# Optimization experiments

Measured on AMD Instinct MI355X. Metric: run time of the kernel, lower is better.

## Reference

```python
import jax, jax.numpy as jnp
import numpy as np

NUM_STEPS = 3  # matches init_kwargs num_steps
UNITS = 256
N_STRUCT = 4096
N_ATOMS_TOTAL = 131072
FEAT_IN = 256


def setup_inputs() -> dict:
    key = jax.random.key(0)
    ks = jax.random.split(key, 7)
    field = jax.random.normal(ks[0], (N_ATOMS_TOTAL, FEAT_IN), dtype=jnp.float32)
    # Dense(units) params
    Wd = jax.random.normal(ks[1], (FEAT_IN, UNITS), dtype=jnp.float32) / np.sqrt(FEAT_IN)
    bd = jnp.zeros((UNITS,), dtype=jnp.float32)
    # Keras LSTM params: kernel [2*units, 4*units], recurrent [units, 4*units], bias [4*units]
    Wk = jax.random.normal(ks[2], (2 * UNITS, 4 * UNITS), dtype=jnp.float32) / np.sqrt(2 * UNITS)
    Wr = jax.random.normal(ks[3], (UNITS, 4 * UNITS), dtype=jnp.float32) / np.sqrt(UNITS)
    b_lstm = jnp.zeros((4 * UNITS,), dtype=jnp.float32)
    # sorted segment ids = get_segment_indices_from_n(counts)
    segment_ids = jnp.sort(jax.random.randint(ks[4], (N_ATOMS_TOTAL,), 0, N_STRUCT)).astype(jnp.int32)
    return {"field": field, "Wd": Wd, "bd": bd, "Wk": Wk, "Wr": Wr,
            "b_lstm": b_lstm, "segment_ids": segment_ids, "n_struct": N_STRUCT}


def _segment_softmax(e, seg, num_segments):
    # per-channel softmax within each segment (matches unsorted_segment_softmax)
    m = jax.ops.segment_max(e, seg, num_segments=num_segments)
    ex = jnp.exp(e - m[seg])
    s = jax.ops.segment_sum(ex, seg, num_segments=num_segments)
    return ex / s[seg]


def _lstm_step(x, h, c, Wk, Wr, b):
    # Keras gate order: i, f, g(c), o
    z = x @ Wk + h @ Wr + b
    i, f, g, o = jnp.split(z, 4, axis=-1)
    c_new = jax.nn.sigmoid(f) * c + jax.nn.sigmoid(i) * jnp.tanh(g)
    h_new = jax.nn.sigmoid(o) * jnp.tanh(c_new)
    return h_new, c_new


def reference(field, Wd, bd, Wk, Wr, b_lstm, segment_ids, n_struct):
    units = Wd.shape[1]
    x = field @ Wd + bd                              # [N_atoms, units]
    q_star = jnp.zeros((n_struct, 2 * units), dtype=x.dtype)
    h = jnp.zeros((n_struct, units), dtype=x.dtype)
    c = jnp.zeros((n_struct, units), dtype=x.dtype)
    for _ in range(NUM_STEPS):
        h, c = _lstm_step(q_star, h, c, Wk, Wr, b_lstm)
        qt = h                                        # [n_struct, units]
        eit = x * qt[segment_ids]                     # gather == tf.repeat(qt, counts)
        ait = _segment_softmax(eit, segment_ids, n_struct)
        rt = jax.ops.segment_sum(ait * x, segment_ids, num_segments=n_struct)
        q_star = jnp.concatenate([qt, rt], axis=-1)   # [n_struct, 2*units]
    return q_star
```

## Files before the change

kernel.cpp:

```cpp
#include <hip/hip_runtime.h>
#include <math.h>

#define N_ATOMS   131072
#define FEAT      256
#define UNITS     256
#define NSTRUCT   4096
#define ZDIM      1024
#define QDIM      512
#define KLSTM     768

typedef __attribute__((ext_vector_type(8))) __bf16 bf16x8;
typedef __attribute__((ext_vector_type(4))) float  f32x4;

__device__ __forceinline__ float sigm(float v) { return 1.0f / (1.0f + __expf(-v)); }

__device__ __forceinline__ unsigned short bf16_rne(float v) {
    unsigned int u = __float_as_uint(v);
    u += 0x7fffu + ((u >> 16) & 1u);
    return (unsigned short)(u >> 16);
}
__device__ __forceinline__ float bf16_f32(unsigned short b) {
    return __uint_as_float(((unsigned int)b) << 16);
}
__device__ __forceinline__ bf16x8 frag_ld(const unsigned short* p) {
    uint4 u = *(const uint4*)p;
    bf16x8 r; __builtin_memcpy(&r, &u, 16); return r;
}

__global__ void seg_offs_kernel(const int* __restrict__ seg, int* __restrict__ offs) {
    int s = blockIdx.x * blockDim.x + threadIdx.x;
    if (s > NSTRUCT) return;
    int lo = 0, hi = N_ATOMS;
    while (lo < hi) {
        int mid = (lo + hi) >> 1;
        if (seg[mid] < s) lo = mid + 1; else hi = mid;
    }
    offs[s] = lo;
}

__global__ __launch_bounds__(256) void prep_wd_kernel(
    const float* __restrict__ Wd, unsigned short* __restrict__ Th,
    unsigned short* __restrict__ Tl)
{
    int t = blockIdx.x * 256 + threadIdx.x;
    int k = t >> 8, n = t & 255;
    float v = Wd[t];
    unsigned short h = bf16_rne(v);
    unsigned short l = bf16_rne(v - bf16_f32(h));
    Th[n * FEAT + k] = h;
    Tl[n * FEAT + k] = l;
}

__global__ __launch_bounds__(256) void prep_wlstm_kernel(
    const float* __restrict__ Wk, const float* __restrict__ Wr,
    unsigned short* __restrict__ Th, unsigned short* __restrict__ Tl)
{
    int t = blockIdx.x * 256 + threadIdx.x;
    int k = t >> 10, n = t & 1023;
    float v = (k < QDIM) ? Wk[t] : Wr[t - QDIM * ZDIM];
    unsigned short h = bf16_rne(v);
    unsigned short l = bf16_rne(v - bf16_f32(h));
    Th[n * KLSTM + k] = h;
    Tl[n * KLSTM + k] = l;
}

__global__ __launch_bounds__(256) void gemm_x_mfma(
    const float* __restrict__ A,
    const unsigned short* __restrict__ BTh,
    const unsigned short* __restrict__ BTl,
    const float* __restrict__ bias, float* __restrict__ C)
{
    __shared__ unsigned short Ah[128][32], Al[128][32], Bh[128][32], Bl[128][32];
    const int bn = blockIdx.x * 128;
    const int bm = blockIdx.y * 128;
    const int t  = threadIdx.x;
    const int w  = t >> 6, l = t & 63;
    const int wr = w & 1, wc = w >> 1;
    const int lm = l & 15, koff = (l >> 4) * 8;

    f32x4 acc[4][4] = {};

    for (int k0 = 0; k0 < FEAT; k0 += 32) {
        #pragma unroll
        for (int i = 0; i < 4; ++i) {
            int flat = t + i * 256;
            int m = flat >> 3, kq = flat & 7;
            const float4 v = *(const float4*)&A[(size_t)(bm + m) * FEAT + k0 + kq * 4];
            unsigned short h0 = bf16_rne(v.x), h1 = bf16_rne(v.y);
            unsigned short h2 = bf16_rne(v.z), h3 = bf16_rne(v.w);
            unsigned short l0 = bf16_rne(v.x - bf16_f32(h0));
            unsigned short l1 = bf16_rne(v.y - bf16_f32(h1));
            unsigned short l2 = bf16_rne(v.z - bf16_f32(h2));
            unsigned short l3 = bf16_rne(v.w - bf16_f32(h3));
            uint2 hw, lw;
            hw.x = (unsigned)h0 | ((unsigned)h1 << 16);
            hw.y = (unsigned)h2 | ((unsigned)h3 << 16);
            lw.x = (unsigned)l0 | ((unsigned)l1 << 16);
            lw.y = (unsigned)l2 | ((unsigned)l3 << 16);
            *(uint2*)&Ah[m][kq * 4] = hw;
            *(uint2*)&Al[m][kq * 4] = lw;
        }
        #pragma unroll
        for (int i = 0; i < 2; ++i) {
            int flat = t + i * 256;
            int n = flat >> 2, kc = flat & 3;
            *(uint4*)&Bh[n][kc * 8] = *(const uint4*)&BTh[(size_t)(bn + n) * FEAT + k0 + kc * 8];
            *(uint4*)&Bl[n][kc * 8] = *(const uint4*)&BTl[(size_t)(bn + n) * FEAT + k0 + kc * 8];
        }
        __syncthreads();
        bf16x8 ah[4], al[4];
        #pragma unroll
        for (int i = 0; i < 4; ++i) {
            ah[i] = frag_ld(&Ah[wr * 64 + i * 16 + lm][koff]);
            al[i] = frag_ld(&Al[wr * 64 + i * 16 + lm][koff]);
        }
        #pragma unroll
        for (int j = 0; j < 4; ++j) {
            bf16x8 bh = frag_ld(&Bh[wc * 64 + j * 16 + lm][koff]);
            bf16x8 bl = frag_ld(&Bl[wc * 64 + j * 16 + lm][koff]);
            #pragma unroll
            for (int i = 0; i < 4; ++i) {
                acc[i][j] = __builtin_amdgcn_mfma_f32_16x16x32_bf16(ah[i], bh, acc[i][j], 0, 0, 0);
                acc[i][j] = __builtin_amdgcn_mfma_f32_16x16x32_bf16(al[i], bh, acc[i][j], 0, 0, 0);
                acc[i][j] = __builtin_amdgcn_mfma_f32_16x16x32_bf16(ah[i], bl, acc[i][j], 0, 0, 0);
            }
        }
        __syncthreads();
    }

    const int lg4 = (l >> 4) * 4;
    #pragma unroll
    for (int i = 0; i < 4; ++i)
        #pragma unroll
        for (int j = 0; j < 4; ++j) {
            int col  = bn + wc * 64 + j * 16 + lm;
            int row0 = bm + wr * 64 + i * 16 + lg4;
            float bb = bias[col];
            #pragma unroll
            for (int r = 0; r < 4; ++r)
                C[(size_t)(row0 + r) * FEAT + col] = acc[i][j][r] + bb;
        }
}

__global__ __launch_bounds__(256) void lstm_gemm_mfma(
    const float* __restrict__ qstar, const float* __restrict__ hsrc,
    const unsigned short* __restrict__ BTh,
    const unsigned short* __restrict__ BTl,
    const float* __restrict__ bias, float* __restrict__ z)
{
    __shared__ unsigned short Ah[128][32], Al[128][32], Bh[128][32], Bl[128][32];
    const int bn = blockIdx.x * 128;
    const int bm = blockIdx.y * 128;
    const int t  = threadIdx.x;
    const int w  = t >> 6, l = t & 63;
    const int wr = w & 1, wc = w >> 1;
    const int lm = l & 15, koff = (l >> 4) * 8;

    f32x4 acc[4][4] = {};

    for (int k0 = 0; k0 < KLSTM; k0 += 32) {
        const float* Asrc; int lda, kb;
        if (k0 < QDIM) { Asrc = qstar; lda = QDIM;  kb = k0; }
        else           { Asrc = hsrc;  lda = UNITS; kb = k0 - QDIM; }
        #pragma unroll
        for (int i = 0; i < 4; ++i) {
            int flat = t + i * 256;
            int m = flat >> 3, kq = flat & 7;
            const float4 v = *(const float4*)&Asrc[(size_t)(bm + m) * lda + kb + kq * 4];
            unsigned short h0 = bf16_rne(v.x), h1 = bf16_rne(v.y);
            unsigned short h2 = bf16_rne(v.z), h3 = bf16_rne(v.w);
            unsigned short l0 = bf16_rne(v.x - bf16_f32(h0));
            unsigned short l1 = bf16_rne(v.y - bf16_f32(h1));
            unsigned short l2 = bf16_rne(v.z - bf16_f32(h2));
            unsigned short l3 = bf16_rne(v.w - bf16_f32(h3));
            uint2 hw, lw;
            hw.x = (unsigned)h0 | ((unsigned)h1 << 16);
            hw.y = (unsigned)h2 | ((unsigned)h3 << 16);
            lw.x = (unsigned)l0 | ((unsigned)l1 << 16);
            lw.y = (unsigned)l2 | ((unsigned)l3 << 16);
            *(uint2*)&Ah[m][kq * 4] = hw;
            *(uint2*)&Al[m][kq * 4] = lw;
        }
        #pragma unroll
        for (int i = 0; i < 2; ++i) {
            int flat = t + i * 256;
            int n = flat >> 2, kc = flat & 3;
            *(uint4*)&Bh[n][kc * 8] = *(const uint4*)&BTh[(size_t)(bn + n) * KLSTM + k0 + kc * 8];
            *(uint4*)&Bl[n][kc * 8] = *(const uint4*)&BTl[(size_t)(bn + n) * KLSTM + k0 + kc * 8];
        }
        __syncthreads();
        bf16x8 ah[4], al[4];
        #pragma unroll
        for (int i = 0; i < 4; ++i) {
            ah[i] = frag_ld(&Ah[wr * 64 + i * 16 + lm][koff]);
            al[i] = frag_ld(&Al[wr * 64 + i * 16 + lm][koff]);
        }
        #pragma unroll
        for (int j = 0; j < 4; ++j) {
            bf16x8 bh = frag_ld(&Bh[wc * 64 + j * 16 + lm][koff]);
            bf16x8 bl = frag_ld(&Bl[wc * 64 + j * 16 + lm][koff]);
            #pragma unroll
            for (int i = 0; i < 4; ++i) {
                acc[i][j] = __builtin_amdgcn_mfma_f32_16x16x32_bf16(ah[i], bh, acc[i][j], 0, 0, 0);
                acc[i][j] = __builtin_amdgcn_mfma_f32_16x16x32_bf16(al[i], bh, acc[i][j], 0, 0, 0);
                acc[i][j] = __builtin_amdgcn_mfma_f32_16x16x32_bf16(ah[i], bl, acc[i][j], 0, 0, 0);
            }
        }
        __syncthreads();
    }

    const int lg4 = (l >> 4) * 4;
    #pragma unroll
    for (int i = 0; i < 4; ++i)
        #pragma unroll
        for (int j = 0; j < 4; ++j) {
            int col  = bn + wc * 64 + j * 16 + lm;
            int row0 = bm + wr * 64 + i * 16 + lg4;
            float bb = bias[col];
            #pragma unroll
            for (int r = 0; r < 4; ++r)
                z[(size_t)(row0 + r) * ZDIM + col] = acc[i][j][r] + bb;
        }
}

__global__ __launch_bounds__(256) void gates_kernel(
    const float* __restrict__ z, const float* __restrict__ c_in,
    float* __restrict__ h_out, float* __restrict__ c_out)
{
    int idx = blockIdx.x * 256 + threadIdx.x;
    int s = idx >> 8, ch = idx & 255;
    const float* zr = z + (size_t)s * ZDIM;
    float zi = zr[ch], zf = zr[256 + ch], zg = zr[512 + ch], zo = zr[768 + ch];
    float cold = c_in[idx];
    float cn = sigm(zf) * cold + sigm(zi) * tanhf(zg);
    float hn = sigm(zo) * tanhf(cn);
    h_out[idx] = hn;
    c_out[idx] = cn;
}

__global__ void h1c1_kernel(const float* __restrict__ b, float* __restrict__ hc_rows) {
    int ch = threadIdx.x;
    float zi = b[ch], zg = b[512 + ch], zo = b[768 + ch];
    float cn = sigm(zi) * tanhf(zg);
    float hn = sigm(zo) * tanhf(cn);
    hc_rows[ch] = hn;
    hc_rows[256 + ch] = cn;
}

__global__ __launch_bounds__(256) void bcast_kernel(
    const float* __restrict__ hc_rows, float* __restrict__ h, float* __restrict__ c)
{
    int idx = blockIdx.x * 256 + threadIdx.x;
    int ch = idx & 255;
    h[idx] = hc_rows[ch];
    c[idx] = hc_rows[256 + ch];
}

__global__ __launch_bounds__(256) void attn_kernel(
    const float* __restrict__ x, const float* __restrict__ h,
    const int* __restrict__ offs, float* __restrict__ qstar_out)
{
    const int s = blockIdx.x;
    const int ch = threadIdx.x;
    const float q = h[(size_t)s * UNITS + ch];
    const int a0 = offs[s], a1 = offs[s + 1];

    float m = -INFINITY, ssum = 0.0f, r = 0.0f;
    #pragma unroll 4
    for (int a = a0; a < a1; ++a) {
        float xv = x[(size_t)a * FEAT + ch];
        float e = xv * q;
        float mnew = fmaxf(m, e);
        float scale = __expf(m - mnew);
        float p = __expf(e - mnew);
        ssum = ssum * scale + p;
        r = r * scale + p * xv;
        m = mnew;
    }
    float rt = (a1 > a0) ? (r / ssum) : 0.0f;
    qstar_out[(size_t)s * QDIM + ch] = q;
    qstar_out[(size_t)s * QDIM + UNITS + ch] = rt;
}

extern "C" void kernel_launch(void* const* d_in, const int* in_sizes, int n_in,
                              void* d_out, int out_size, void* d_ws, size_t ws_size,
                              hipStream_t stream) {
    const float* field  = (const float*)d_in[0];
    const float* Wd     = (const float*)d_in[1];
    const float* bd     = (const float*)d_in[2];
    const float* Wk     = (const float*)d_in[3];
    const float* Wr     = (const float*)d_in[4];
    const float* b_lstm = (const float*)d_in[5];
    const int*   segids = (const int*)d_in[6];

    float* ws   = (float*)d_ws;
    float* x    = ws;
    float* z    = x + (size_t)N_ATOMS * FEAT;
    float* qst  = z + (size_t)NSTRUCT * ZDIM;
    float* h    = qst + (size_t)NSTRUCT * QDIM;
    float* c    = h + (size_t)NSTRUCT * UNITS;
    float* hcr  = c + (size_t)NSTRUCT * UNITS;
    int*   offs = (int*)(hcr + 512);

    unsigned short* wdt_h = (unsigned short*)d_out;
    unsigned short* wdt_l = wdt_h + 256 * 256;
    unsigned short* wt_h  = wdt_l + 256 * 256;
    unsigned short* wt_l  = wt_h + 1024 * 768;

    seg_offs_kernel<<<(NSTRUCT + 1 + 255) / 256, 256, 0, stream>>>(segids, offs);
    prep_wd_kernel<<<256, 256, 0, stream>>>(Wd, wdt_h, wdt_l);
    prep_wlstm_kernel<<<3072, 256, 0, stream>>>(Wk, Wr, wt_h, wt_l);

    gemm_x_mfma<<<dim3(FEAT / 128, N_ATOMS / 128), 256, 0, stream>>>(
        field, wdt_h, wdt_l, bd, x);

    h1c1_kernel<<<1, 256, 0, stream>>>(b_lstm, hcr);
    bcast_kernel<<<NSTRUCT, 256, 0, stream>>>(hcr, h, c);
    attn_kernel<<<NSTRUCT, 256, 0, stream>>>(x, h, offs, qst);

    for (int step = 1; step < 3; ++step) {
        lstm_gemm_mfma<<<dim3(ZDIM / 128, NSTRUCT / 128), 256, 0, stream>>>(
            qst, h, wt_h, wt_l, b_lstm, z);
        gates_kernel<<<NSTRUCT, 256, 0, stream>>>(z, c, h, c);
        float* qdst = (step == 2) ? (float*)d_out : qst;
        attn_kernel<<<NSTRUCT, 256, 0, stream>>>(x, h, offs, qdst);
    }
}
```

Before: 441.1 us.

## Widen x-projection GEMM tile to full N, pad LDS, batch attention softmax

The field projection GEMM now computes all 256 output columns per block, so each 128-row A tile is loaded and split into bf16 hi/lo only once instead of twice. LDS rows in both GEMMs are padded from 32 to 40 elements to reduce bank conflicts. The attention online softmax processes four atoms per iteration with one rescale, cutting the exp and dependency chain. The wider tile doubles accumulator registers, which may lower occupancy.

```diff
diff --git a/kernel.cpp b/kernel.cpp
--- a/kernel.cpp
+++ b/kernel.cpp
@@ -64,21 +64,22 @@
     Tl[n * KLSTM + k] = l;
 }
 
+#define LDP 40
 __global__ __launch_bounds__(256) void gemm_x_mfma(
     const float* __restrict__ A,
     const unsigned short* __restrict__ BTh,
     const unsigned short* __restrict__ BTl,
     const float* __restrict__ bias, float* __restrict__ C)
 {
-    __shared__ unsigned short Ah[128][32], Al[128][32], Bh[128][32], Bl[128][32];
-    const int bn = blockIdx.x * 128;
-    const int bm = blockIdx.y * 128;
+    __shared__ unsigned short Ah[128][LDP], Al[128][LDP];
+    __shared__ unsigned short Bh[256][LDP], Bl[256][LDP];
+    const int bm = blockIdx.x * 128;
     const int t  = threadIdx.x;
     const int w  = t >> 6, l = t & 63;
     const int wr = w & 1, wc = w >> 1;
     const int lm = l & 15, koff = (l >> 4) * 8;
 
-    f32x4 acc[4][4] = {};
+    f32x4 acc[4][8] = {};
 
     for (int k0 = 0; k0 < FEAT; k0 += 32) {
         #pragma unroll
@@ -101,11 +102,11 @@
             *(uint2*)&Al[m][kq * 4] = lw;
         }
         #pragma unroll
-        for (int i = 0; i < 2; ++i) {
+        for (int i = 0; i < 4; ++i) {
             int flat = t + i * 256;
             int n = flat >> 2, kc = flat & 3;
-            *(uint4*)&Bh[n][kc * 8] = *(const uint4*)&BTh[(size_t)(bn + n) * FEAT + k0 + kc * 8];
-            *(uint4*)&Bl[n][kc * 8] = *(const uint4*)&BTl[(size_t)(bn + n) * FEAT + k0 + kc * 8];
+            *(uint4*)&Bh[n][kc * 8] = *(const uint4*)&BTh[(size_t)n * FEAT + k0 + kc * 8];
+            *(uint4*)&Bl[n][kc * 8] = *(const uint4*)&BTl[(size_t)n * FEAT + k0 + kc * 8];
         }
         __syncthreads();
         bf16x8 ah[4], al[4];
@@ -115,9 +116,9 @@
             al[i] = frag_ld(&Al[wr * 64 + i * 16 + lm][koff]);
         }
         #pragma unroll
-        for (int j = 0; j < 4; ++j) {
-            bf16x8 bh = frag_ld(&Bh[wc * 64 + j * 16 + lm][koff]);
-            bf16x8 bl = frag_ld(&Bl[wc * 64 + j * 16 + lm][koff]);
+        for (int j = 0; j < 8; ++j) {
+            bf16x8 bh = frag_ld(&Bh[wc * 128 + j * 16 + lm][koff]);
+            bf16x8 bl = frag_ld(&Bl[wc * 128 + j * 16 + lm][koff]);
             #pragma unroll
             for (int i = 0; i < 4; ++i) {
                 acc[i][j] = __builtin_amdgcn_mfma_f32_16x16x32_bf16(ah[i], bh, acc[i][j], 0, 0, 0);
@@ -132,8 +133,8 @@
     #pragma unroll
     for (int i = 0; i < 4; ++i)
         #pragma unroll
-        for (int j = 0; j < 4; ++j) {
-            int col  = bn + wc * 64 + j * 16 + lm;
+        for (int j = 0; j < 8; ++j) {
+            int col  = wc * 128 + j * 16 + lm;
             int row0 = bm + wr * 64 + i * 16 + lg4;
             float bb = bias[col];
             #pragma unroll
@@ -148,7 +149,8 @@
     const unsigned short* __restrict__ BTl,
     const float* __restrict__ bias, float* __restrict__ z)
 {
-    __shared__ unsigned short Ah[128][32], Al[128][32], Bh[128][32], Bl[128][32];
+    __shared__ unsigned short Ah[128][LDP], Al[128][LDP];
+    __shared__ unsigned short Bh[128][LDP], Bl[128][LDP];
     const int bn = blockIdx.x * 128;
     const int bm = blockIdx.y * 128;
     const int t  = threadIdx.x;
@@ -266,16 +268,30 @@
     const int a0 = offs[s], a1 = offs[s + 1];
 
     float m = -INFINITY, ssum = 0.0f, r = 0.0f;
-    #pragma unroll 4
-    for (int a = a0; a < a1; ++a) {
+    int a = a0;
+    for (; a + 3 < a1; a += 4) {
+        float x0 = x[(size_t)(a + 0) * FEAT + ch];
+        float x1 = x[(size_t)(a + 1) * FEAT + ch];
+        float x2 = x[(size_t)(a + 2) * FEAT + ch];
+        float x3 = x[(size_t)(a + 3) * FEAT + ch];
+        float e0 = x0 * q, e1 = x1 * q, e2 = x2 * q, e3 = x3 * q;
+        float mn = fmaxf(fmaxf(fmaxf(e0, e1), fmaxf(e2, e3)), m);
+        float sc = __expf(m - mn);
+        float p0 = __expf(e0 - mn), p1 = __expf(e1 - mn);
+        float p2 = __expf(e2 - mn), p3 = __expf(e3 - mn);
+        ssum = ssum * sc + ((p0 + p1) + (p2 + p3));
+        r    = r    * sc + ((p0 * x0 + p1 * x1) + (p2 * x2 + p3 * x3));
+        m = mn;
+    }
+    for (; a < a1; ++a) {
         float xv = x[(size_t)a * FEAT + ch];
         float e = xv * q;
-        float mnew = fmaxf(m, e);
-        float scale = __expf(m - mnew);
-        float p = __expf(e - mnew);
-        ssum = ssum * scale + p;
-        r = r * scale + p * xv;
-        m = mnew;
+        float mn = fmaxf(m, e);
+        float sc = __expf(m - mn);
+        float p = __expf(e - mn);
+        ssum = ssum * sc + p;
+        r = r * sc + p * xv;
+        m = mn;
     }
     float rt = (a1 > a0) ? (r / ssum) : 0.0f;
     qstar_out[(size_t)s * QDIM + ch] = q;
@@ -311,8 +327,7 @@
     prep_wd_kernel<<<256, 256, 0, stream>>>(Wd, wdt_h, wdt_l);
     prep_wlstm_kernel<<<3072, 256, 0, stream>>>(Wk, Wr, wt_h, wt_l);
 
-    gemm_x_mfma<<<dim3(FEAT / 128, N_ATOMS / 128), 256, 0, stream>>>(
-        field, wdt_h, wdt_l, bd, x);
+    gemm_x_mfma<<<N_ATOMS / 128, 256, 0, stream>>>(field, wdt_h, wdt_l, bd, x);
 
     h1c1_kernel<<<1, 256, 0, stream>>>(b_lstm, hcr);
     bcast_kernel<<<NSTRUCT, 256, 0, stream>>>(hcr, h, c);
```

After: 449.3 us. About the same (+1.8%).

## Split attention over four atom partitions and pad GEMM LDS rows

Applied to the files above, without the earlier changes.

The attention kernel now uses 1024 threads per structure. Four partitions each run an online softmax over interleaved atoms, four loads at a time, and the partial max/sum/weighted sums are merged through shared memory. This targets the latency of the serial dependency chain in the per-segment loop. Separately, both MFMA GEMMs pad their LDS tiles from 32 to 40 columns to reduce bank conflicts on fragment loads, and issue the B-tile loads before the A conversion. The changes cost more shared memory and a block-level sync, and three quarters of the threads sit idle during the final merge.

```diff
diff --git a/kernel.cpp b/kernel.cpp
--- a/kernel.cpp
+++ b/kernel.cpp
@@ -8,6 +8,7 @@
 #define ZDIM      1024
 #define QDIM      512
 #define KLSTM     768
+#define LDP       40
 
 typedef __attribute__((ext_vector_type(8))) __bf16 bf16x8;
 typedef __attribute__((ext_vector_type(4))) float  f32x4;
@@ -70,7 +71,8 @@
     const unsigned short* __restrict__ BTl,
     const float* __restrict__ bias, float* __restrict__ C)
 {
-    __shared__ unsigned short Ah[128][32], Al[128][32], Bh[128][32], Bl[128][32];
+    __shared__ unsigned short Ah[128][LDP], Al[128][LDP];
+    __shared__ unsigned short Bh[128][LDP], Bl[128][LDP];
     const int bn = blockIdx.x * 128;
     const int bm = blockIdx.y * 128;
     const int t  = threadIdx.x;
@@ -81,6 +83,13 @@
     f32x4 acc[4][4] = {};
 
     for (int k0 = 0; k0 < FEAT; k0 += 32) {
+        #pragma unroll
+        for (int i = 0; i < 2; ++i) {
+            int flat = t + i * 256;
+            int n = flat >> 2, kc = flat & 3;
+            *(uint4*)&Bh[n][kc * 8] = *(const uint4*)&BTh[(size_t)(bn + n) * FEAT + k0 + kc * 8];
+            *(uint4*)&Bl[n][kc * 8] = *(const uint4*)&BTl[(size_t)(bn + n) * FEAT + k0 + kc * 8];
+        }
         #pragma unroll
         for (int i = 0; i < 4; ++i) {
             int flat = t + i * 256;
@@ -100,13 +109,6 @@
             *(uint2*)&Ah[m][kq * 4] = hw;
             *(uint2*)&Al[m][kq * 4] = lw;
         }
-        #pragma unroll
-        for (int i = 0; i < 2; ++i) {
-            int flat = t + i * 256;
-            int n = flat >> 2, kc = flat & 3;
-            *(uint4*)&Bh[n][kc * 8] = *(const uint4*)&BTh[(size_t)(bn + n) * FEAT + k0 + kc * 8];
-            *(uint4*)&Bl[n][kc * 8] = *(const uint4*)&BTl[(size_t)(bn + n) * FEAT + k0 + kc * 8];
-        }
         __syncthreads();
         bf16x8 ah[4], al[4];
         #pragma unroll
@@ -148,7 +150,8 @@
     const unsigned short* __restrict__ BTl,
     const float* __restrict__ bias, float* __restrict__ z)
 {
-    __shared__ unsigned short Ah[128][32], Al[128][32], Bh[128][32], Bl[128][32];
+    __shared__ unsigned short Ah[128][LDP], Al[128][LDP];
+    __shared__ unsigned short Bh[128][LDP], Bl[128][LDP];
     const int bn = blockIdx.x * 128;
     const int bm = blockIdx.y * 128;
     const int t  = threadIdx.x;
@@ -159,6 +162,13 @@
     f32x4 acc[4][4] = {};
 
     for (int k0 = 0; k0 < KLSTM; k0 += 32) {
+        #pragma unroll
+        for (int i = 0; i < 2; ++i) {
+            int flat = t + i * 256;
+            int n = flat >> 2, kc = flat & 3;
+            *(uint4*)&Bh[n][kc * 8] = *(const uint4*)&BTh[(size_t)(bn + n) * KLSTM + k0 + kc * 8];
+            *(uint4*)&Bl[n][kc * 8] = *(const uint4*)&BTl[(size_t)(bn + n) * KLSTM + k0 + kc * 8];
+        }
         const float* Asrc; int lda, kb;
         if (k0 < QDIM) { Asrc = qstar; lda = QDIM;  kb = k0; }
         else           { Asrc = hsrc;  lda = UNITS; kb = k0 - QDIM; }
@@ -181,13 +191,6 @@
             *(uint2*)&Ah[m][kq * 4] = hw;
             *(uint2*)&Al[m][kq * 4] = lw;
         }
-        #pragma unroll
-        for (int i = 0; i < 2; ++i) {
-            int flat = t + i * 256;
-            int n = flat >> 2, kc = flat & 3;
-            *(uint4*)&Bh[n][kc * 8] = *(const uint4*)&BTh[(size_t)(bn + n) * KLSTM + k0 + kc * 8];
-            *(uint4*)&Bl[n][kc * 8] = *(const uint4*)&BTl[(size_t)(bn + n) * KLSTM + k0 + kc * 8];
-        }
         __syncthreads();
         bf16x8 ah[4], al[4];
         #pragma unroll
@@ -256,30 +259,61 @@
     c[idx] = hc_rows[256 + ch];
 }
 
-__global__ __launch_bounds__(256) void attn_kernel(
+__global__ __launch_bounds__(1024) void attn_kernel(
     const float* __restrict__ x, const float* __restrict__ h,
     const int* __restrict__ offs, float* __restrict__ qstar_out)
 {
-    const int s = blockIdx.x;
-    const int ch = threadIdx.x;
+    __shared__ float Lm[4][UNITS], Ls[4][UNITS], Lr[4][UNITS];
+    const int s  = blockIdx.x;
+    const int t  = threadIdx.x;
+    const int ch = t & 255;
+    const int p  = t >> 8;
     const float q = h[(size_t)s * UNITS + ch];
     const int a0 = offs[s], a1 = offs[s + 1];
 
     float m = -INFINITY, ssum = 0.0f, r = 0.0f;
-    #pragma unroll 4
-    for (int a = a0; a < a1; ++a) {
+    int a = a0 + p;
+    for (; a + 12 < a1; a += 16) {
+        float x0 = x[(size_t)(a +  0) * FEAT + ch];
+        float x1 = x[(size_t)(a +  4) * FEAT + ch];
+        float x2 = x[(size_t)(a +  8) * FEAT + ch];
+        float x3 = x[(size_t)(a + 12) * FEAT + ch];
+        float e0 = x0 * q, e1 = x1 * q, e2 = x2 * q, e3 = x3 * q;
+        float mn = fmaxf(fmaxf(fmaxf(e0, e1), fmaxf(e2, e3)), m);
+        float sc = __expf(m - mn);
+        float p0 = __expf(e0 - mn), p1 = __expf(e1 - mn);
+        float p2 = __expf(e2 - mn), p3 = __expf(e3 - mn);
+        ssum = ssum * sc + ((p0 + p1) + (p2 + p3));
+        r    = r    * sc + ((p0 * x0 + p1 * x1) + (p2 * x2 + p3 * x3));
+        m = mn;
+    }
+    for (; a < a1; a += 4) {
         float xv = x[(size_t)a * FEAT + ch];
         float e = xv * q;
-        float mnew = fmaxf(m, e);
-        float scale = __expf(m - mnew);
-        float p = __expf(e - mnew);
-        ssum = ssum * scale + p;
-        r = r * scale + p * xv;
-        m = mnew;
-    }
-    float rt = (a1 > a0) ? (r / ssum) : 0.0f;
-    qstar_out[(size_t)s * QDIM + ch] = q;
-    qstar_out[(size_t)s * QDIM + UNITS + ch] = rt;
+        float mn = fmaxf(m, e);
+        float sc = __expf(m - mn);
+        float pe = __expf(e - mn);
+        ssum = ssum * sc + pe;
+        r = r * sc + pe * xv;
+        m = mn;
+    }
+    Lm[p][ch] = m; Ls[p][ch] = ssum; Lr[p][ch] = r;
+    __syncthreads();
+
+    if (p == 0) {
+        float m0 = Lm[0][ch], m1 = Lm[1][ch], m2 = Lm[2][ch], m3 = Lm[3][ch];
+        float ms = fmaxf(fmaxf(m0, m1), fmaxf(m2, m3));
+        float rt = 0.0f;
+        if (a1 > a0) {
+            float w0 = __expf(m0 - ms), w1 = __expf(m1 - ms);
+            float w2 = __expf(m2 - ms), w3 = __expf(m3 - ms);
+            float S = Ls[0][ch] * w0 + Ls[1][ch] * w1 + Ls[2][ch] * w2 + Ls[3][ch] * w3;
+            float R = Lr[0][ch] * w0 + Lr[1][ch] * w1 + Lr[2][ch] * w2 + Lr[3][ch] * w3;
+            rt = R / S;
+        }
+        qstar_out[(size_t)s * QDIM + ch] = q;
+        qstar_out[(size_t)s * QDIM + UNITS + ch] = rt;
+    }
 }
 
 extern "C" void kernel_launch(void* const* d_in, const int* in_sizes, int n_in,
@@ -316,13 +350,13 @@
 
     h1c1_kernel<<<1, 256, 0, stream>>>(b_lstm, hcr);
     bcast_kernel<<<NSTRUCT, 256, 0, stream>>>(hcr, h, c);
-    attn_kernel<<<NSTRUCT, 256, 0, stream>>>(x, h, offs, qst);
+    attn_kernel<<<NSTRUCT, 1024, 0, stream>>>(x, h, offs, qst);
 
     for (int step = 1; step < 3; ++step) {
         lstm_gemm_mfma<<<dim3(ZDIM / 128, NSTRUCT / 128), 256, 0, stream>>>(
             qst, h, wt_h, wt_l, b_lstm, z);
         gates_kernel<<<NSTRUCT, 256, 0, stream>>>(z, c, h, c);
         float* qdst = (step == 2) ? (float*)d_out : qst;
-        attn_kernel<<<NSTRUCT, 256, 0, stream>>>(x, h, offs, qdst);
-    }
-}
+        attn_kernel<<<NSTRUCT, 1024, 0, stream>>>(x, h, offs, qdst);
+    }
+}
```

After: 447.5 us. About the same (+1.4%).
